# Kernel tuning notes

Measured on AMD Instinct MI355X. Metric: run time of the kernel, lower is better.

## Reference

```python
import jax, jax.numpy as jnp
import numpy as np

N_HEAD = 16

def setup_inputs() -> dict:
    key = jax.random.key(0)
    k1, k2, k3 = jax.random.split(key, 3)
    B, T, C = 2, 2048, 2048
    x = jax.random.normal(k1, (B, T, C), dtype=jnp.float32)
    # torch Linear weights are [out, in]; init with small scale for stability
    w_attn = jax.random.normal(k2, (3 * C, C), dtype=jnp.float32) * 0.02
    b_attn = jnp.zeros((3 * C,), dtype=jnp.float32)
    w_proj = jax.random.normal(k3, (C, C), dtype=jnp.float32) * 0.02
    b_proj = jnp.zeros((C,), dtype=jnp.float32)
    return {"x": x, "w_attn": w_attn, "b_attn": b_attn, "w_proj": w_proj, "b_proj": b_proj}

def reference(x, w_attn, b_attn, w_proj, b_proj):
    B, T, C = x.shape
    nh = N_HEAD
    hs = C // nh
    # fused QKV projection (torch Linear: x @ W^T + b)
    qkv = x @ w_attn.T + b_attn                      # [B, T, 3C]
    q, k, v = jnp.split(qkv, 3, axis=2)
    # [B, nh, T, hs]
    q = q.reshape(B, T, nh, hs).transpose(0, 2, 1, 3)
    k = k.reshape(B, T, nh, hs).transpose(0, 2, 1, 3)
    v = v.reshape(B, T, nh, hs).transpose(0, 2, 1, 3)
    # causal scaled dot-product attention
    scale = 1.0 / jnp.sqrt(jnp.asarray(hs, dtype=x.dtype))
    logits = jnp.einsum("bhqd,bhkd->bhqk", q, k) * scale  # [B, nh, T, T]
    causal = jnp.tril(jnp.ones((T, T), dtype=bool))
    logits = jnp.where(causal, logits, jnp.finfo(logits.dtype).min)
    attn = jax.nn.softmax(logits, axis=-1)
    y = jnp.einsum("bhqk,bhkd->bhqd", attn, v)       # [B, nh, T, hs]
    y = y.transpose(0, 2, 1, 3).reshape(B, T, C)
    # output projection (resid_dropout is identity in eval / p=0)
    y = y @ w_proj.T + b_proj
    return y
```

## Files before the change

### kernel.cpp

```cpp
#include <hip/hip_runtime.h>
#include <stdint.h>

typedef __bf16 bf16_t;
typedef __bf16 bf16x8 __attribute__((ext_vector_type(8)));
typedef float f32x4 __attribute__((ext_vector_type(4)));
typedef unsigned short us16x8 __attribute__((ext_vector_type(8)));

#define MFMA16(a, b, c) __builtin_amdgcn_mfma_f32_16x16x32_bf16(a, b, c, 0, 0, 0)
#define BAR() __builtin_amdgcn_s_barrier()
#define PRIO1() __builtin_amdgcn_s_setprio(1)
#define PRIO0() __builtin_amdgcn_s_setprio(0)
#define LGKM0()                                       \
  do {                                                \
    asm volatile("s_waitcnt lgkmcnt(0)" ::: "memory"); \
    __builtin_amdgcn_sched_barrier(0);                \
  } while (0)
#define VMCNT(n)                                             \
  do {                                                       \
    asm volatile("s_waitcnt vmcnt(" #n ")" ::: "memory");    \
    __builtin_amdgcn_sched_barrier(0);                       \
  } while (0)

__device__ __forceinline__ void stage16(const bf16_t* g, bf16_t* l) {
  __builtin_amdgcn_global_load_lds((__attribute__((address_space(1))) void*)g,
                                   (__attribute__((address_space(3))) void*)l, 16, 0, 0);
}

__global__ __launch_bounds__(256) void cvt_f32_to_bf16(const float* __restrict__ in,
                                                       bf16_t* __restrict__ out, int n8) {
  int i = blockIdx.x * 256 + threadIdx.x;
  if (i >= n8) return;
  const f32x4* p = (const f32x4*)(in + (size_t)i * 8);
  f32x4 a = p[0], b = p[1];
  bf16x8 o;
  o[0] = (bf16_t)a[0]; o[1] = (bf16_t)a[1]; o[2] = (bf16_t)a[2]; o[3] = (bf16_t)a[3];
  o[4] = (bf16_t)b[0]; o[5] = (bf16_t)b[1]; o[6] = (bf16_t)b[2]; o[7] = (bf16_t)b[3];
  *(bf16x8*)(out + (size_t)i * 8) = o;
}

struct G8P {
  const bf16_t* Ab;
  const bf16_t* Bb;
  bf16_t* SA;
  bf16_t* SB;
  int K, nk, tid, ardBase, brdBase, pb0, pb1;
};

__device__ __forceinline__ void stage_half(const bf16_t* src, bf16_t* dst, int K) {
  stage16(src, dst);
  stage16(src + ((size_t)K << 6), dst + 4096);
}

template <int CUR>
__device__ __forceinline__ void g8p_group(const G8P& g, int t, bf16x8 (&aR)[4][2],
                                          bf16x8 (&bR0)[2][2], bf16x8 (&bR1)[2][2],
                                          f32x4 (&acc)[8][4]) {
  const int t1 = (t + 1 < g.nk) ? t + 1 : g.nk - 1;
  const int t2 = (t + 2 < g.nk) ? t + 2 : g.nk - 1;
  bf16_t* SAc = g.SA + CUR * 16384;
  bf16_t* SBc = g.SB + CUR * 16384;
  bf16_t* SAn = g.SA + (1 - CUR) * 16384;

#pragma unroll
  for (int mi = 0; mi < 4; ++mi) {
    aR[mi][0] = *(const bf16x8*)(SAc + g.ardBase + mi * 1024 + g.pb0);
    aR[mi][1] = *(const bf16x8*)(SAc + g.ardBase + mi * 1024 + g.pb1);
  }
#pragma unroll
  for (int ni = 0; ni < 2; ++ni) {
    bR0[ni][0] = *(const bf16x8*)(SBc + g.brdBase + ni * 1024 + g.pb0);
    bR0[ni][1] = *(const bf16x8*)(SBc + g.brdBase + ni * 1024 + g.pb1);
  }
  stage_half(g.Ab + (size_t)128 * g.K + (size_t)t1 * 64, SAn + 8192 + g.tid * 8, g.K);
  BAR();
  LGKM0();
  PRIO1();
#pragma unroll
  for (int mi = 0; mi < 4; ++mi)
#pragma unroll
    for (int ni = 0; ni < 2; ++ni) {
      acc[mi][ni] = MFMA16(aR[mi][0], bR0[ni][0], acc[mi][ni]);
      acc[mi][ni] = MFMA16(aR[mi][1], bR0[ni][1], acc[mi][ni]);
    }
  PRIO0();
  BAR();

#pragma unroll
  for (int ni = 0; ni < 2; ++ni) {
    bR1[ni][0] = *(const bf16x8*)(SBc + g.brdBase + (2 + ni) * 1024 + g.pb0);
    bR1[ni][1] = *(const bf16x8*)(SBc + g.brdBase + (2 + ni) * 1024 + g.pb1);
  }
  BAR();
  LGKM0();
  PRIO1();
#pragma unroll
  for (int mi = 0; mi < 4; ++mi)
#pragma unroll
    for (int ni = 0; ni < 2; ++ni) {
      acc[mi][2 + ni] = MFMA16(aR[mi][0], bR1[ni][0], acc[mi][2 + ni]);
      acc[mi][2 + ni] = MFMA16(aR[mi][1], bR1[ni][1], acc[mi][2 + ni]);
    }
  PRIO0();
  BAR();

#pragma unroll
  for (int mi = 0; mi < 4; ++mi) {
    aR[mi][0] = *(const bf16x8*)(SAc + g.ardBase + (4 + mi) * 1024 + g.pb0);
    aR[mi][1] = *(const bf16x8*)(SAc + g.ardBase + (4 + mi) * 1024 + g.pb1);
  }
  stage_half(g.Bb + (size_t)t2 * 64, SBc + g.tid * 8, g.K);
  BAR();
  LGKM0();
  PRIO1();
#pragma unroll
  for (int mi = 0; mi < 4; ++mi)
#pragma unroll
    for (int ni = 0; ni < 2; ++ni) {
      acc[4 + mi][2 + ni] = MFMA16(aR[mi][0], bR1[ni][0], acc[4 + mi][2 + ni]);
      acc[4 + mi][2 + ni] = MFMA16(aR[mi][1], bR1[ni][1], acc[4 + mi][2 + ni]);
    }
  PRIO0();
  BAR();

  stage_half(g.Ab + (size_t)t2 * 64, SAc + g.tid * 8, g.K);
  stage_half(g.Bb + (size_t)128 * g.K + (size_t)t2 * 64, SBc + 8192 + g.tid * 8, g.K);
  VMCNT(6);
  BAR();
  PRIO1();
#pragma unroll
  for (int mi = 0; mi < 4; ++mi)
#pragma unroll
    for (int ni = 0; ni < 2; ++ni) {
      acc[4 + mi][ni] = MFMA16(aR[mi][0], bR0[ni][0], acc[4 + mi][ni]);
      acc[4 + mi][ni] = MFMA16(aR[mi][1], bR0[ni][1], acc[4 + mi][ni]);
    }
  PRIO0();
  BAR();
}

__global__ __launch_bounds__(512, 2) void gemm_nt_8p(const bf16_t* __restrict__ A,
                                                     const bf16_t* __restrict__ B,
                                                     const float* __restrict__ bias,
                                                     bf16_t* __restrict__ C,
                                                     int M, int N, int K) {
  __shared__ bf16_t SA[2 * 256 * 64];
  __shared__ bf16_t SB[2 * 256 * 64];
  int tid = threadIdx.x;
  int l = tid & 63, w = tid >> 6;
  int l15 = l & 15, l4 = l >> 4, l7 = l & 7;
  int wm = w >> 2, wn = w & 3;
  int nbn = N >> 8;
  int nwg = gridDim.x;
  int bid = blockIdx.x;
  int wg = (bid & 7) * (nwg >> 3) + (bid >> 3);
  int bm = wg / nbn, bn = wg % nbn;

  int row0 = tid >> 3;
  int swc0 = ((tid & 7) ^ (row0 & 7)) << 3;
  G8P g;
  g.Ab = A + (size_t)(bm * 256 + row0) * K + swc0;
  g.Bb = B + (size_t)(bn * 256 + row0) * K + swc0;
  g.SA = SA; g.SB = SB;
  g.K = K; g.nk = K >> 6; g.tid = tid;
  g.ardBase = (wm * 128 + l15) * 64;
  g.brdBase = (wn * 64 + l15) * 64;
  g.pb0 = ((l4) ^ l7) << 3;
  g.pb1 = ((4 + l4) ^ l7) << 3;

  f32x4 acc[8][4] = {};
  bf16x8 aR[4][2], bR0[2][2], bR1[2][2];

  {
    int t1 = (g.nk > 1) ? 1 : 0;
    stage_half(g.Ab, SA + tid * 8, K);
    stage_half(g.Bb, SB + tid * 8, K);
    stage_half(g.Bb + (size_t)128 * K, SB + 8192 + tid * 8, K);
    stage_half(g.Ab + (size_t)128 * K, SA + 8192 + tid * 8, K);
    stage_half(g.Ab + (size_t)t1 * 64, SA + 16384 + tid * 8, K);
    stage_half(g.Bb + (size_t)t1 * 64, SB + 16384 + tid * 8, K);
    stage_half(g.Bb + (size_t)128 * K + (size_t)t1 * 64, SB + 16384 + 8192 + tid * 8, K);
    VMCNT(6);
    BAR();
  }

  for (int t = 0; t < g.nk; t += 2) {
    g8p_group<0>(g, t, aR, bR0, bR1, acc);
    g8p_group<1>(g, t + 1, aR, bR0, bR1, acc);
  }
  asm volatile("s_waitcnt vmcnt(0)" ::: "memory");

  int rbase = bm * 256 + wm * 128 + (l4 << 2);
  int cbase = bn * 256 + wn * 64 + l15;
#pragma unroll
  for (int ni = 0; ni < 4; ++ni) {
    float bv = bias[cbase + ni * 16];
#pragma unroll
    for (int mi = 0; mi < 8; ++mi)
#pragma unroll
      for (int r = 0; r < 4; ++r) {
        size_t off = (size_t)(rbase + mi * 16 + r) * N + (cbase + ni * 16);
        C[off] = (bf16_t)(acc[mi][ni][r] + bv);
      }
  }
}

template <int OUT_BF16>
__global__ __launch_bounds__(256) void gemm_nt(const bf16_t* __restrict__ A,
                                               const bf16_t* __restrict__ B,
                                               const float* __restrict__ bias,
                                               void* __restrict__ Cout,
                                               int M, int N, int K) {
  __shared__ bf16_t As[128 * 64];
  __shared__ bf16_t Bs[128 * 64];
  int tid = threadIdx.x;
  int l = tid & 63, w = tid >> 6;
  int wr = w >> 1, wc = w & 1;
  int nbn = N >> 7;
  int bm = blockIdx.x / nbn, bn = blockIdx.x % nbn;
  int l15 = l & 15, l4 = l >> 4, l7 = l & 7;

  f32x4 acc[4][4] = {};

  for (int ks = 0; ks < K; ks += 64) {
#pragma unroll
    for (int i = 0; i < 4; ++i) {
      int e = i * 256 + tid;
      int row = e >> 3, blk = e & 7;
      int col = ks + ((blk ^ (row & 7)) << 3);
      stage16(A + (size_t)(bm * 128 + row) * K + col, As + e * 8);
      stage16(B + (size_t)(bn * 128 + row) * K + col, Bs + e * 8);
    }
    __syncthreads();
#pragma unroll
    for (int kk = 0; kk < 2; ++kk) {
      bf16x8 af[4], bfr[4];
      int blk = (kk * 4 + l4) ^ l7;
#pragma unroll
      for (int m = 0; m < 4; ++m) {
        af[m] = *(const bf16x8*)(As + (wr * 64 + m * 16 + l15) * 64 + blk * 8);
        bfr[m] = *(const bf16x8*)(Bs + (wc * 64 + m * 16 + l15) * 64 + blk * 8);
      }
#pragma unroll
      for (int m = 0; m < 4; ++m)
#pragma unroll
        for (int n = 0; n < 4; ++n)
          acc[m][n] = MFMA16(af[m], bfr[n], acc[m][n]);
    }
    __syncthreads();
  }

  int rbase = bm * 128 + wr * 64 + (l4 << 2);
  int cbase = bn * 128 + wc * 64 + l15;
#pragma unroll
  for (int n = 0; n < 4; ++n) {
    float bv = bias[cbase + n * 16];
#pragma unroll
    for (int m = 0; m < 4; ++m)
#pragma unroll
      for (int r = 0; r < 4; ++r) {
        float v = acc[m][n][r] + bv;
        size_t off = (size_t)(rbase + m * 16 + r) * N + (cbase + n * 16);
        if (OUT_BF16) ((bf16_t*)Cout)[off] = (bf16_t)v;
        else ((float*)Cout)[off] = v;
      }
  }
}

__global__ __launch_bounds__(256, 2) void attn_fwd(const bf16_t* __restrict__ qkv,
                                                   bf16_t* __restrict__ att) {
  __shared__ bf16_t Kt[64 * 128];
  __shared__ bf16_t Vt[128 * 64];
  __shared__ bf16_t Pw[4][16 * 64];

  int bid = blockIdx.x;
  int pair = bid >> 5, bh = bid & 31;
  int h = bh & 15, b = bh >> 4;
  int tid = threadIdx.x;
  int l = tid & 63, w = tid >> 6;
  int l15 = l & 15, l4 = l >> 4, l7 = l & 7;
  const size_t LD = 6144;
  const bf16_t* base = qkv + (size_t)b * 2048 * LD;

#pragma unroll 1
  for (int phase = 0; phase < 2; ++phase) {
    int qt = phase ? 31 - pair : pair;
    int q0 = qt << 6;
    int wq0 = q0 + w * 16;

    bf16x8 qf[4];
#pragma unroll
    for (int kk = 0; kk < 4; ++kk)
      qf[kk] = *(const bf16x8*)(base + (size_t)(wq0 + l15) * LD + h * 128 + kk * 32 + l4 * 8);

    f32x4 acc[8] = {};
    float mrow[4], lrow[4];
#pragma unroll
    for (int r = 0; r < 4; ++r) { mrow[r] = -1e30f; lrow[r] = 0.f; }

    int nkt = qt + 1;
    for (int kt = 0; kt < nkt; ++kt) {
      int kb = kt << 6;
      const bf16_t* vg = base + (size_t)kb * LD + 4096 + h * 128;
      us16x8 va[2], vb[2];
#pragma unroll
      for (int p = 0; p < 2; ++p) {
        int g = p * 256 + tid;
        int kv = (g >> 4) << 1;
        int d0 = (g & 15) << 3;
        va[p] = *(const us16x8*)(vg + (size_t)kv * LD + d0);
        vb[p] = *(const us16x8*)(vg + (size_t)(kv + 1) * LD + d0);
      }
      const bf16_t* kg = base + (size_t)kb * LD + 2048 + h * 128;
#pragma unroll
      for (int i = 0; i < 4; ++i) {
        int e = i * 256 + tid;
        int row = e >> 4, blk = e & 15;
        int src = (blk ^ (row & 7)) << 3;
        stage16(kg + (size_t)row * LD + src, Kt + e * 8);
      }
#pragma unroll
      for (int p = 0; p < 2; ++p) {
        int g = p * 256 + tid;
        int kv = (g >> 4) << 1;
        int d0 = (g & 15) << 3;
        int k8 = kv >> 3, kr = kv & 7;
#pragma unroll
        for (int j = 0; j < 8; ++j) {
          int d = d0 + j;
          int swz = k8 ^ ((d ^ (d >> 3)) & 7);
          unsigned pack = (unsigned)va[p][j] | ((unsigned)vb[p][j] << 16);
          *(unsigned*)(&Vt[d * 64 + swz * 8 + kr]) = pack;
        }
      }
      __syncthreads();

      {
        f32x4 s[4] = {};
        __builtin_amdgcn_s_setprio(1);
#pragma unroll
        for (int kk = 0; kk < 4; ++kk) {
          int blk = (kk * 4 + l4) ^ l7;
#pragma unroll
          for (int n = 0; n < 4; ++n) {
            bf16x8 kf = *(const bf16x8*)(Kt + (n * 16 + l15) * 128 + blk * 8);
            s[n] = MFMA16(qf[kk], kf, s[n]);
          }
        }
        __builtin_amdgcn_s_setprio(0);

        const float sc = 0.08838834764831845f;
        bool needMask = (kb + 63) > wq0;
        float scf[4];
#pragma unroll
        for (int r = 0; r < 4; ++r) {
          int q = wq0 + (l4 << 2) + r;
#pragma unroll
          for (int n = 0; n < 4; ++n) {
            float v = s[n][r] * sc;
            if (needMask && (kb + n * 16 + l15) > q) v = -1e30f;
            s[n][r] = v;
          }
          float mx = fmaxf(fmaxf(s[0][r], s[1][r]), fmaxf(s[2][r], s[3][r]));
          mx = fmaxf(mx, __shfl_xor(mx, 1));
          mx = fmaxf(mx, __shfl_xor(mx, 2));
          mx = fmaxf(mx, __shfl_xor(mx, 4));
          mx = fmaxf(mx, __shfl_xor(mx, 8));
          float mn = fmaxf(mrow[r], mx);
          float sf = __expf(mrow[r] - mn);
          mrow[r] = mn;
          scf[r] = sf;
          float rs = 0.f;
#pragma unroll
          for (int n = 0; n < 4; ++n) {
            float pv = __expf(s[n][r] - mn);
            s[n][r] = pv;
            rs += pv;
          }
          rs += __shfl_xor(rs, 1);
          rs += __shfl_xor(rs, 2);
          rs += __shfl_xor(rs, 4);
          rs += __shfl_xor(rs, 8);
          lrow[r] = lrow[r] * sf + rs;
        }
#pragma unroll
        for (int nd = 0; nd < 8; ++nd)
#pragma unroll
          for (int r = 0; r < 4; ++r)
            acc[nd][r] *= scf[r];
#pragma unroll
        for (int n = 0; n < 4; ++n) {
          int cb8 = n * 2 + (l15 >> 3);
#pragma unroll
          for (int r = 0; r < 4; ++r) {
            int row = (l4 << 2) + r;
            Pw[w][row * 64 + ((cb8 ^ (row & 7)) << 3) + l7] = (bf16_t)s[n][r];
          }
        }
        __builtin_amdgcn_s_setprio(1);
#pragma unroll
        for (int kk2 = 0; kk2 < 2; ++kk2) {
          bf16x8 pa = *(const bf16x8*)(&Pw[w][l15 * 64 + (((kk2 * 4 + l4) ^ l7) << 3)]);
#pragma unroll
          for (int nd = 0; nd < 8; ++nd) {
            int d = nd * 16 + l15;
            int swz = (kk2 * 4 + l4) ^ ((d ^ (d >> 3)) & 7);
            bf16x8 bv = *(const bf16x8*)(&Vt[d * 64 + swz * 8]);
            acc[nd] = MFMA16(pa, bv, acc[nd]);
          }
        }
        __builtin_amdgcn_s_setprio(0);
      }
      __syncthreads();
    }

#pragma unroll
    for (int r = 0; r < 4; ++r) {
      float inv = 1.0f / lrow[r];
      size_t ro = (size_t)(b * 2048 + wq0 + (l4 << 2) + r) * 2048 + h * 128;
#pragma unroll
      for (int nd = 0; nd < 8; ++nd)
        att[ro + nd * 16 + l15] = (bf16_t)(acc[nd][r] * inv);
    }
  }
}

extern "C" void kernel_launch(void* const* d_in, const int* in_sizes, int n_in,
                              void* d_out, int out_size, void* d_ws, size_t ws_size,
                              hipStream_t stream) {
  (void)in_sizes; (void)n_in; (void)out_size; (void)ws_size;
  const float* x = (const float*)d_in[0];
  const float* w_attn = (const float*)d_in[1];
  const float* b_attn = (const float*)d_in[2];
  const float* w_proj = (const float*)d_in[3];
  const float* b_proj = (const float*)d_in[4];
  float* out = (float*)d_out;

  char* ws = (char*)d_ws;
  bf16_t* xb  = (bf16_t*)(ws);
  bf16_t* wab = (bf16_t*)(ws + 16777216);
  bf16_t* wpb = (bf16_t*)(ws + 41943040);
  bf16_t* qkv = (bf16_t*)(ws + 50331648);
  bf16_t* att = xb;

  cvt_f32_to_bf16<<<4096, 256, 0, stream>>>(x, xb, 1048576);
  cvt_f32_to_bf16<<<6144, 256, 0, stream>>>(w_attn, wab, 1572864);
  cvt_f32_to_bf16<<<2048, 256, 0, stream>>>(w_proj, wpb, 524288);

  gemm_nt_8p<<<384, 512, 0, stream>>>(xb, wab, b_attn, qkv, 4096, 6144, 2048);

  attn_fwd<<<512, 256, 0, stream>>>(qkv, att);

  gemm_nt<0><<<32 * 16, 256, 0, stream>>>(att, wpb, b_proj, out, 4096, 2048, 2048);
}
```

Measured before the change: 294.6 us.

## Split QKV GEMM into waves, add pipelined 256x128 GEMM, skip masked attention tiles

The QKV projection is split so the Q/K columns run on the 256x256 8-wave kernel over exactly 256 tiles, and the V columns run on a new triple-buffered 256x128 persistent GEMM. The same new GEMM replaces the simple 128x128 output-projection kernel. The goal is to remove the partial-wave tail of the 384-block launch and to give the output projection better prefetching and data reuse. Attention also skips QK/PV compute for key blocks that fall entirely above the causal diagonal for a wave's queries. This adds one kernel launch.

Result: slower. 317.3 us (+7.7%).

```diff
diff --git a/kernel.cpp b/kernel.cpp
--- a/kernel.cpp
+++ b/kernel.cpp
@@ -10,15 +10,15 @@
 #define BAR() __builtin_amdgcn_s_barrier()
 #define PRIO1() __builtin_amdgcn_s_setprio(1)
 #define PRIO0() __builtin_amdgcn_s_setprio(0)
-#define LGKM0()                                       \
-  do {                                                \
+#define LGKM0()                                        \
+  do {                                                 \
     asm volatile("s_waitcnt lgkmcnt(0)" ::: "memory"); \
-    __builtin_amdgcn_sched_barrier(0);                \
+    __builtin_amdgcn_sched_barrier(0);                 \
   } while (0)
-#define VMCNT(n)                                             \
-  do {                                                       \
-    asm volatile("s_waitcnt vmcnt(" #n ")" ::: "memory");    \
-    __builtin_amdgcn_sched_barrier(0);                       \
+#define VMCNT(n)                                          \
+  do {                                                    \
+    asm volatile("s_waitcnt vmcnt(" #n ")" ::: "memory"); \
+    __builtin_amdgcn_sched_barrier(0);                    \
   } while (0)
 
 __device__ __forceinline__ void stage16(const bf16_t* g, bf16_t* l) {
@@ -142,14 +142,15 @@
                                                      const bf16_t* __restrict__ B,
                                                      const float* __restrict__ bias,
                                                      bf16_t* __restrict__ C,
-                                                     int M, int N, int K) {
+                                                     int M, int Ncols, int Nstride,
+                                                     int K) {
   __shared__ bf16_t SA[2 * 256 * 64];
   __shared__ bf16_t SB[2 * 256 * 64];
   int tid = threadIdx.x;
   int l = tid & 63, w = tid >> 6;
   int l15 = l & 15, l4 = l >> 4, l7 = l & 7;
   int wm = w >> 2, wn = w & 3;
-  int nbn = N >> 8;
+  int nbn = Ncols >> 8;
   int nwg = gridDim.x;
   int bid = blockIdx.x;
   int wg = (bid & 7) * (nwg >> 3) + (bid >> 3);
@@ -198,71 +199,112 @@
     for (int mi = 0; mi < 8; ++mi)
 #pragma unroll
       for (int r = 0; r < 4; ++r) {
-        size_t off = (size_t)(rbase + mi * 16 + r) * N + (cbase + ni * 16);
+        size_t off = (size_t)(rbase + mi * 16 + r) * Nstride + (cbase + ni * 16);
         C[off] = (bf16_t)(acc[mi][ni][r] + bv);
       }
   }
 }
 
 template <int OUT_BF16>
-__global__ __launch_bounds__(256) void gemm_nt(const bf16_t* __restrict__ A,
-                                               const bf16_t* __restrict__ B,
-                                               const float* __restrict__ bias,
-                                               void* __restrict__ Cout,
-                                               int M, int N, int K) {
-  __shared__ bf16_t As[128 * 64];
-  __shared__ bf16_t Bs[128 * 64];
-  int tid = threadIdx.x;
-  int l = tid & 63, w = tid >> 6;
-  int wr = w >> 1, wc = w & 1;
-  int nbn = N >> 7;
-  int bm = blockIdx.x / nbn, bn = blockIdx.x % nbn;
-  int l15 = l & 15, l4 = l >> 4, l7 = l & 7;
-
-  f32x4 acc[4][4] = {};
-
-  for (int ks = 0; ks < K; ks += 64) {
-#pragma unroll
-    for (int i = 0; i < 4; ++i) {
-      int e = i * 256 + tid;
-      int row = e >> 3, blk = e & 7;
-      int col = ks + ((blk ^ (row & 7)) << 3);
-      stage16(A + (size_t)(bm * 128 + row) * K + col, As + e * 8);
-      stage16(B + (size_t)(bn * 128 + row) * K + col, Bs + e * 8);
-    }
-    __syncthreads();
-#pragma unroll
-    for (int kk = 0; kk < 2; ++kk) {
-      bf16x8 af[4], bfr[4];
-      int blk = (kk * 4 + l4) ^ l7;
-#pragma unroll
-      for (int m = 0; m < 4; ++m) {
-        af[m] = *(const bf16x8*)(As + (wr * 64 + m * 16 + l15) * 64 + blk * 8);
-        bfr[m] = *(const bf16x8*)(Bs + (wc * 64 + m * 16 + l15) * 64 + blk * 8);
-      }
-#pragma unroll
-      for (int m = 0; m < 4; ++m)
-#pragma unroll
-        for (int n = 0; n < 4; ++n)
-          acc[m][n] = MFMA16(af[m], bfr[n], acc[m][n]);
-    }
-    __syncthreads();
-  }
-
-  int rbase = bm * 128 + wr * 64 + (l4 << 2);
-  int cbase = bn * 128 + wc * 64 + l15;
-#pragma unroll
-  for (int n = 0; n < 4; ++n) {
-    float bv = bias[cbase + n * 16];
-#pragma unroll
-    for (int m = 0; m < 4; ++m)
-#pragma unroll
-      for (int r = 0; r < 4; ++r) {
-        float v = acc[m][n][r] + bv;
-        size_t off = (size_t)(rbase + m * 16 + r) * N + (cbase + n * 16);
-        if (OUT_BF16) ((bf16_t*)Cout)[off] = (bf16_t)v;
-        else ((float*)Cout)[off] = v;
-      }
+__global__ __launch_bounds__(256, 2) void gemm_w128p(const bf16_t* __restrict__ A,
+                                                     const bf16_t* __restrict__ B,
+                                                     const float* __restrict__ bias,
+                                                     void* __restrict__ Cout,
+                                                     int M, int N, int K,
+                                                     int Nstride, int ncol0) {
+  __shared__ bf16_t SA[3 * 256 * 32];
+  __shared__ bf16_t SB[3 * 128 * 32];
+  const int tid = threadIdx.x;
+  const int l = tid & 63, w = tid >> 6;
+  const int l15 = l & 15, l4 = l >> 4;
+  const int wm = w >> 1, wn = w & 1;
+  const int nbn = N >> 7;
+  const int nbm = M >> 8;
+  const int total = nbm * nbn;
+  const int bnpc = nbn >> 3;
+
+  const int r0 = tid >> 2;
+  const int scol = (((tid & 3) ^ ((r0 >> 1) & 3)) << 3);
+  const size_t K64 = (size_t)64 * K;
+
+  const int swz = (l4 ^ ((l15 >> 1) & 3)) << 3;
+  int aoff[8], boff[4];
+#pragma unroll
+  for (int i = 0; i < 8; ++i) aoff[i] = (wm * 128 + i * 16 + l15) * 32 + swz;
+#pragma unroll
+  for (int i = 0; i < 4; ++i) boff[i] = (wn * 64 + i * 16 + l15) * 32 + swz;
+
+  const int nk = K >> 5;
+
+  for (int wk = blockIdx.x; wk < total; wk += gridDim.x) {
+    const int c = wk & 7, rr0 = wk >> 3;
+    const int bm = rr0 / bnpc;
+    const int bn = c * bnpc + rr0 % bnpc;
+
+    const bf16_t* gA = A + (size_t)(bm * 256 + r0) * K + scol;
+    const bf16_t* gB = B + (size_t)(bn * 128 + r0) * K + scol;
+
+    f32x4 acc[8][4] = {};
+
+    auto STAGE = [&](int t2, int buf) {
+      const size_t ko = (size_t)t2 * 32;
+      stage16(gA + ko, SA + buf * 8192 + tid * 8);
+      stage16(gA + K64 + ko, SA + buf * 8192 + 2048 + tid * 8);
+      stage16(gA + 2 * K64 + ko, SA + buf * 8192 + 4096 + tid * 8);
+      stage16(gA + 3 * K64 + ko, SA + buf * 8192 + 6144 + tid * 8);
+      stage16(gB + ko, SB + buf * 4096 + tid * 8);
+      stage16(gB + K64 + ko, SB + buf * 4096 + 2048 + tid * 8);
+    };
+
+    auto TILE = [&](int t, int bufR, int bufS) {
+      const int t2 = (t + 2 < nk) ? t + 2 : nk - 1;
+      STAGE(t2, bufS);
+      bf16x8 aR[8], bR[4];
+#pragma unroll
+      for (int i = 0; i < 8; ++i) aR[i] = *(const bf16x8*)(SA + bufR * 8192 + aoff[i]);
+#pragma unroll
+      for (int i = 0; i < 4; ++i) bR[i] = *(const bf16x8*)(SB + bufR * 4096 + boff[i]);
+      VMCNT(6);
+      BAR();
+      LGKM0();
+      PRIO1();
+#pragma unroll
+      for (int mi = 0; mi < 8; ++mi)
+#pragma unroll
+        for (int ni = 0; ni < 4; ++ni)
+          acc[mi][ni] = MFMA16(aR[mi], bR[ni], acc[mi][ni]);
+      PRIO0();
+      BAR();
+    };
+
+    STAGE(0, 0);
+    STAGE(1, 1);
+    VMCNT(6);
+    BAR();
+
+    for (int t = 0; t < nk - 1; t += 3) {
+      TILE(t, 0, 2);
+      TILE(t + 1, 1, 0);
+      TILE(t + 2, 2, 1);
+    }
+    TILE(nk - 1, 0, 2);
+    VMCNT(0);
+
+    const int rbase = bm * 256 + wm * 128 + (l4 << 2);
+    const int cbase = bn * 128 + wn * 64 + l15;
+#pragma unroll
+    for (int ni = 0; ni < 4; ++ni) {
+      float bv = bias[cbase + ni * 16];
+#pragma unroll
+      for (int mi = 0; mi < 8; ++mi)
+#pragma unroll
+        for (int rr = 0; rr < 4; ++rr) {
+          float v = acc[mi][ni][rr] + bv;
+          size_t off = (size_t)(rbase + mi * 16 + rr) * Nstride + (ncol0 + cbase + ni * 16);
+          if (OUT_BF16) ((bf16_t*)Cout)[off] = (bf16_t)v;
+          else ((float*)Cout)[off] = v;
+        }
+    }
   }
 }
 
@@ -327,16 +369,17 @@
 #pragma unroll
         for (int j = 0; j < 8; ++j) {
           int d = d0 + j;
-          int swz = k8 ^ ((d ^ (d >> 3)) & 7);
+          int swzv = k8 ^ ((d ^ (d >> 3)) & 7);
           unsigned pack = (unsigned)va[p][j] | ((unsigned)vb[p][j] << 16);
-          *(unsigned*)(&Vt[d * 64 + swz * 8 + kr]) = pack;
+          *(unsigned*)(&Vt[d * 64 + swzv * 8 + kr]) = pack;
         }
       }
       __syncthreads();
 
-      {
+      if (kb < wq0 + 32) {
+        bool needMask = (kb + 63) > wq0;
         f32x4 s[4] = {};
-        __builtin_amdgcn_s_setprio(1);
+        PRIO1();
 #pragma unroll
         for (int kk = 0; kk < 4; ++kk) {
           int blk = (kk * 4 + l4) ^ l7;
@@ -346,10 +389,9 @@
             s[n] = MFMA16(qf[kk], kf, s[n]);
           }
         }
-        __builtin_amdgcn_s_setprio(0);
+        PRIO0();
 
         const float sc = 0.08838834764831845f;
-        bool needMask = (kb + 63) > wq0;
         float scf[4];
 #pragma unroll
         for (int r = 0; r < 4; ++r) {
@@ -396,19 +438,19 @@
             Pw[w][row * 64 + ((cb8 ^ (row & 7)) << 3) + l7] = (bf16_t)s[n][r];
           }
         }
-        __builtin_amdgcn_s_setprio(1);
+        PRIO1();
 #pragma unroll
         for (int kk2 = 0; kk2 < 2; ++kk2) {
           bf16x8 pa = *(const bf16x8*)(&Pw[w][l15 * 64 + (((kk2 * 4 + l4) ^ l7) << 3)]);
 #pragma unroll
           for (int nd = 0; nd < 8; ++nd) {
             int d = nd * 16 + l15;
-            int swz = (kk2 * 4 + l4) ^ ((d ^ (d >> 3)) & 7);
-            bf16x8 bv = *(const bf16x8*)(&Vt[d * 64 + swz * 8]);
+            int swzv = (kk2 * 4 + l4) ^ ((d ^ (d >> 3)) & 7);
+            bf16x8 bv = *(const bf16x8*)(&Vt[d * 64 + swzv * 8]);
             acc[nd] = MFMA16(pa, bv, acc[nd]);
           }
         }
-        __builtin_amdgcn_s_setprio(0);
+        PRIO0();
       }
       __syncthreads();
     }
@@ -446,9 +488,11 @@
   cvt_f32_to_bf16<<<6144, 256, 0, stream>>>(w_attn, wab, 1572864);
   cvt_f32_to_bf16<<<2048, 256, 0, stream>>>(w_proj, wpb, 524288);
 
-  gemm_nt_8p<<<384, 512, 0, stream>>>(xb, wab, b_attn, qkv, 4096, 6144, 2048);
+  gemm_nt_8p<<<256, 512, 0, stream>>>(xb, wab, b_attn, qkv, 4096, 4096, 6144, 2048);
+  gemm_w128p<1><<<256, 256, 0, stream>>>(xb, wab + (size_t)4096 * 2048, b_attn + 4096,
+                                         qkv, 4096, 2048, 2048, 6144, 4096);
 
   attn_fwd<<<512, 256, 0, stream>>>(qkv, att);
 
-  gemm_nt<0><<<32 * 16, 256, 0, stream>>>(att, wpb, b_proj, out, 4096, 2048, 2048);
-}
+  gemm_w128p<0><<<512, 256, 0, stream>>>(att, wpb, b_proj, out, 4096, 2048, 2048, 2048, 0);
+}
```
